# Kernel optimization log

Hardware: AMD Instinct MI355X
Metric: run time of the kernel (lower is better)

Reference implementation:

```python
import jax, jax.numpy as jnp
import numpy as np

N_NODES = 50000
N_EDGES = 800000
NUM_GRAPHS = 64
NEG_SLOPE = 0.2


def gatv2_layer(x, src, dst, Wl, bl, Wr, br, att, b_out, heads, out_ch, concat):
    # PyG GATv2Conv: x_j = lin_l(x)[src], x_i = lin_r(x)[dst]
    N = x.shape[0]
    xl = (x @ Wl + bl).reshape(N, heads, out_ch)
    xr = (x @ Wr + br).reshape(N, heads, out_ch)
    m = xl[src] + xr[dst]                                  # [E, H, C]
    e = jax.nn.leaky_relu(m, negative_slope=NEG_SLOPE)
    logits = jnp.einsum('ehc,hc->eh', e, att)              # [E, H]
    # softmax over incoming edges of each destination node
    seg_max = jax.ops.segment_max(logits, dst, num_segments=N)
    ex = jnp.exp(logits - seg_max[dst])
    denom = jax.ops.segment_sum(ex, dst, num_segments=N)
    alpha = ex / denom[dst]                                # [E, H]
    out = jax.ops.segment_sum(alpha[..., None] * xl[src], dst, num_segments=N)
    out = out.reshape(N, heads * out_ch) if concat else out.mean(axis=1)
    return out + b_out


def _forward(x, edge_index, batch,
             Wl1, bl1, Wr1, br1, att1, b1,
             Wl2, bl2, Wr2, br2, att2, b2,
             Wl3, bl3, Wr3, br3, att3, b3,
             Wm1, bm1, Wm2, bm2):
    N = x.shape[0]
    loops = jnp.arange(N, dtype=edge_index.dtype)
    src = jnp.concatenate([edge_index[0], loops])          # add_self_loops=True
    dst = jnp.concatenate([edge_index[1], loops])
    h = jax.nn.relu(gatv2_layer(x, src, dst, Wl1, bl1, Wr1, br1, att1, b1, 4, 64, True))
    h = jax.nn.relu(gatv2_layer(h, src, dst, Wl2, bl2, Wr2, br2, att2, b2, 2, 64, True))
    h = jax.nn.relu(gatv2_layer(h, src, dst, Wl3, bl3, Wr3, br3, att3, b3, 1, 64, False))
    # global_mean_pool
    sums = jax.ops.segment_sum(h, batch, num_segments=NUM_GRAPHS)
    counts = jax.ops.segment_sum(jnp.ones((N, 1), h.dtype), batch, num_segments=NUM_GRAPHS)
    pooled = sums / jnp.maximum(counts, 1.0)
    return jax.nn.relu(pooled @ Wm1 + bm1) @ Wm2 + bm2


def setup_inputs() -> dict:
    key = jax.random.key(0)
    ks = jax.random.split(key, 24)
    s = 0.05
    inp = {
        'x': jax.random.normal(ks[0], (N_NODES, 128), jnp.float32),
        'edge_index': jax.random.randint(ks[1], (2, N_EDGES), 0, N_NODES, jnp.int64),
        'batch': jnp.sort(jax.random.randint(ks[2], (N_NODES,), 0, NUM_GRAPHS, jnp.int64)),
        # conv1: in=128, heads=4, C=64
        'Wl1': jax.random.normal(ks[3], (128, 256), jnp.float32) * s,
        'bl1': jnp.zeros((256,), jnp.float32),
        'Wr1': jax.random.normal(ks[4], (128, 256), jnp.float32) * s,
        'br1': jnp.zeros((256,), jnp.float32),
        'att1': jax.random.normal(ks[5], (4, 64), jnp.float32) * s,
        'b1': jnp.zeros((256,), jnp.float32),
        # conv2: in=256, heads=2, C=64
        'Wl2': jax.random.normal(ks[6], (256, 128), jnp.float32) * s,
        'bl2': jnp.zeros((128,), jnp.float32),
        'Wr2': jax.random.normal(ks[7], (256, 128), jnp.float32) * s,
        'br2': jnp.zeros((128,), jnp.float32),
        'att2': jax.random.normal(ks[8], (2, 64), jnp.float32) * s,
        'b2': jnp.zeros((128,), jnp.float32),
        # conv3: in=128, heads=1, C=64, concat=False
        'Wl3': jax.random.normal(ks[9], (128, 64), jnp.float32) * s,
        'bl3': jnp.zeros((64,), jnp.float32),
        'Wr3': jax.random.normal(ks[10], (128, 64), jnp.float32) * s,
        'br3': jnp.zeros((64,), jnp.float32),
        'att3': jax.random.normal(ks[11], (1, 64), jnp.float32) * s,
        'b3': jnp.zeros((64,), jnp.float32),
        # MLP 64 -> 32 -> 2
        'Wm1': jax.random.normal(ks[12], (64, 32), jnp.float32) * s,
        'bm1': jnp.zeros((32,), jnp.float32),
        'Wm2': jax.random.normal(ks[13], (32, 2), jnp.float32) * s,
        'bm2': jnp.zeros((2,), jnp.float32),
    }
    return inp


def reference(x, edge_index, batch,
              Wl1, bl1, Wr1, br1, att1, b1,
              Wl2, bl2, Wr2, br2, att2, b2,
              Wl3, bl3, Wr3, br3, att3, b3,
              Wm1, bm1, Wm2, bm2):
    return _forward(x, edge_index, batch,
                    Wl1, bl1, Wr1, br1, att1, b1,
                    Wl2, bl2, Wr2, br2, att2, b2,
                    Wl3, bl3, Wr3, br3, att3, b3,
                    Wm1, bm1, Wm2, bm2)
```

## Files before the change

kernel.cpp:

```cpp
#include <hip/hip_runtime.h>


typedef __attribute__((ext_vector_type(8))) short bf16x8;
typedef __attribute__((ext_vector_type(4))) float f32x4;

#define SORT_BLOCKS 64
#define SCAN_BLOCKS 256

__device__ inline unsigned short f2bf(float f) {
    unsigned u = __float_as_uint(f);
    unsigned r = (u + 0x7fff + ((u >> 16) & 1)) >> 16;
    return (unsigned short)r;
}

__device__ inline void unpack8(uint4 a, float* d) {
    d[0] = __uint_as_float(a.x << 16); d[1] = __uint_as_float(a.x & 0xffff0000u);
    d[2] = __uint_as_float(a.y << 16); d[3] = __uint_as_float(a.y & 0xffff0000u);
    d[4] = __uint_as_float(a.z << 16); d[5] = __uint_as_float(a.z & 0xffff0000u);
    d[6] = __uint_as_float(a.w << 16); d[7] = __uint_as_float(a.w & 0xffff0000u);
}

__global__ __launch_bounds__(256) void prep_kernel(
    const float* __restrict__ x, const int* __restrict__ batch, int N, int K1,
    unsigned short* __restrict__ xb,
    const float* __restrict__ Wl1, const float* __restrict__ Wr1,
    unsigned short* __restrict__ T1l, unsigned short* __restrict__ T1r,
    const float* __restrict__ Wl2, const float* __restrict__ Wr2,
    unsigned short* __restrict__ T2l, unsigned short* __restrict__ T2r,
    const float* __restrict__ Wl3, const float* __restrict__ Wr3,
    unsigned short* __restrict__ T3l, unsigned short* __restrict__ T3r,
    int* __restrict__ deg, int* __restrict__ bound)
{
    const int gtid = blockIdx.x * 256 + threadIdx.x;
    const int gsz = (int)gridDim.x * 256;

    for (int i = gtid; i < N; i += gsz) deg[i] = 0;

    for (int n = gtid; n < N; n += gsz) {
        int bn = batch[n];
        int prev = (n == 0) ? -1 : batch[n - 1];
        for (int g = prev + 1; g <= bn; ++g) bound[g] = n;
        if (n == N - 1)
            for (int g = bn + 1; g <= 64; ++g) bound[g] = N;
    }

    {
        int n4 = (N * K1) >> 2;
        for (int i = gtid; i < n4; i += gsz) {
            float4 v = *reinterpret_cast<const float4*>(x + (size_t)i * 4);
            ushort4 o;
            o.x = f2bf(v.x); o.y = f2bf(v.y); o.z = f2bf(v.z); o.w = f2bf(v.w);
            *reinterpret_cast<ushort4*>(xb + (size_t)i * 4) = o;
        }
    }
    for (int id = gtid; id < 147456; id += gsz) {
        const float* W; unsigned short* T; int K, No, idx;
        if (id < 65536) {
            K = 128; No = 256; idx = id & 32767;
            W = (id < 32768) ? Wl1 : Wr1; T = (id < 32768) ? T1l : T1r;
        } else if (id < 131072) {
            int v = id - 65536; K = 256; No = 128; idx = v & 32767;
            W = (v < 32768) ? Wl2 : Wr2; T = (v < 32768) ? T2l : T2r;
        } else {
            int v = id - 131072; K = 128; No = 64; idx = v & 8191;
            W = (v < 8192) ? Wl3 : Wr3; T = (v < 8192) ? T3l : T3r;
        }
        int n = idx / K, k = idx - n * K;
        T[idx] = f2bf(W[(size_t)k * No + n]);
    }
}

template <int K, int NY>
__global__ __launch_bounds__(256) void gemm_slab(
    const unsigned short* __restrict__ A,
    const unsigned short* __restrict__ W0, const unsigned short* __restrict__ W1,
    const float* __restrict__ bias0, const float* __restrict__ bias1,
    unsigned short* __restrict__ OutL, unsigned short* __restrict__ OutR,
    int M)
{
    constexpr int CPR = K / 8;
    __shared__ __align__(16) char As[64 * K * 2];
    __shared__ __align__(16) char Bs[64 * 128 * 2];

    const int t = threadIdx.x;
    const int lane = t & 63;
    const int wid = t >> 6;
    const int row0 = blockIdx.x * 64;

    #pragma unroll
    for (int i = 0; i < (64 * CPR) / 256; ++i) {
        int c16 = i * 256 + t;
        int r = c16 / CPR, j = c16 % CPR;
        int gr = row0 + r; if (gr > M - 1) gr = M - 1;
        uint4 v = *reinterpret_cast<const uint4*>(A + (size_t)gr * K + j * 8);
        *reinterpret_cast<uint4*>(As + r * (2 * K) + ((j ^ (r & 7)) << 4)) = v;
    }

    const int ra = wid * 16 + (lane & 15);
    const int rowA_byte = ra * (2 * K);

    for (int z = 0; z < 2; ++z) {
        const unsigned short* Wt = z ? W1 : W0;
        const float* bias = z ? bias1 : bias0;
        unsigned short* Out = z ? OutR : OutL;
        for (int y = 0; y < NY; ++y) {
            f32x4 acc[4];
            #pragma unroll
            for (int j = 0; j < 4; ++j) acc[j] = (f32x4){0.f, 0.f, 0.f, 0.f};

            #pragma unroll
            for (int kh = 0; kh < K / 128; ++kh) {
                __syncthreads();
                #pragma unroll
                for (int i = 0; i < 4; ++i) {
                    int c16 = i * 256 + t;
                    int n = c16 >> 4, j = c16 & 15;
                    uint4 v = *reinterpret_cast<const uint4*>(
                        Wt + (size_t)(y * 64 + n) * K + kh * 128 + j * 8);
                    *reinterpret_cast<uint4*>(Bs + n * 256 + ((j ^ (n & 7)) << 4)) = v;
                }
                __syncthreads();
                #pragma unroll
                for (int ks = 0; ks < 4; ++ks) {
                    int chA = kh * 16 + ks * 4 + (lane >> 4);
                    bf16x8 a = *reinterpret_cast<const bf16x8*>(
                        As + rowA_byte + ((chA ^ (ra & 7)) << 4));
                    #pragma unroll
                    for (int j = 0; j < 4; ++j) {
                        int nb = j * 16 + (lane & 15);
                        int chB = ks * 4 + (lane >> 4);
                        bf16x8 b = *reinterpret_cast<const bf16x8*>(
                            Bs + nb * 256 + ((chB ^ (nb & 7)) << 4));
                        acc[j] = __builtin_amdgcn_mfma_f32_16x16x32_bf16(a, b, acc[j], 0, 0, 0);
                    }
                }
            }
            __syncthreads();
            #pragma unroll
            for (int j = 0; j < 4; ++j) {
                float bb = bias[y * 64 + j * 16 + (lane & 15)];
                #pragma unroll
                for (int q = 0; q < 4; ++q) {
                    int r = wid * 16 + (lane >> 4) * 4 + q;
                    int c = j * 16 + (lane & 15);
                    *reinterpret_cast<unsigned short*>(Bs + r * 128 + c * 2)
                        = f2bf(acc[j][q] + bb);
                }
            }
            __syncthreads();
            {
                int r = t >> 2, ch = t & 3;
                int gr = row0 + r;
                if (gr < M) {
                    const uint4* src = reinterpret_cast<const uint4*>(Bs + r * 128 + ch * 32);
                    uint4 v0 = src[0], v1 = src[1];
                    uint4* dst = reinterpret_cast<uint4*>(
                        Out + ((size_t)y * M + gr) * 64 + ch * 16);
                    dst[0] = v0; dst[1] = v1;
                }
            }
        }
    }
}

__global__ void hist_kernel(const int* __restrict__ ei, int E, int Etot,
                            int* __restrict__ deg)
{
    int i = blockIdx.x * blockDim.x + threadIdx.x;
    if (i >= Etot) return;
    int d = (i < E) ? ei[E + i] : (i - E);
    atomicAdd(&deg[d], 1);
}

__global__ __launch_bounds__(256) void scan1_kernel(
    const int* __restrict__ deg, int* __restrict__ blockSums, int N)
{
    __shared__ int red[256];
    const int b = blockIdx.x, t = threadIdx.x;
    const int chunk = (N + SCAN_BLOCKS - 1) / SCAN_BLOCKS;
    const int lo = b * chunk;
    const int hi = (lo + chunk < N) ? lo + chunk : N;
    int s = 0;
    for (int i = lo + t; i < hi; i += 256) s += deg[i];
    red[t] = s;
    __syncthreads();
    #pragma unroll
    for (int off = 128; off > 0; off >>= 1) {
        if (t < off) red[t] += red[t + off];
        __syncthreads();
    }
    if (t == 0) blockSums[b] = red[0];
}

__global__ __launch_bounds__(256) void scan3b_kernel(
    const int* __restrict__ deg, const int* __restrict__ blockSums,
    int* __restrict__ rowptr, int* __restrict__ cursor, int N)
{
    __shared__ int sh[256];
    const int b = blockIdx.x, t = threadIdx.x;
    const int chunk = (N + SCAN_BLOCKS - 1) / SCAN_BLOCKS;
    const int lo = b * chunk;
    const int hi = (lo + chunk < N) ? lo + chunk : N;

    sh[t] = blockSums[t];
    __syncthreads();
    for (int off = 1; off < 256; off <<= 1) {
        int u = (t >= off) ? sh[t - off] : 0;
        __syncthreads();
        sh[t] += u;
        __syncthreads();
    }
    if (b == 0 && t == 255) rowptr[N] = sh[255];
    int carry = (b == 0) ? 0 : sh[b - 1];
    __syncthreads();

    for (int j = lo; j < hi; j += 256) {
        int i = j + t;
        int v = (i < hi) ? deg[i] : 0;
        sh[t] = v;
        __syncthreads();
        for (int off = 1; off < 256; off <<= 1) {
            int u = (t >= off) ? sh[t - off] : 0;
            __syncthreads();
            sh[t] += u;
            __syncthreads();
        }
        int excl = carry + sh[t] - v;
        if (i < hi) { rowptr[i] = excl; cursor[i] = excl; }
        carry += sh[255];
        __syncthreads();
    }
}

__global__ void scatter_kernel(const int* __restrict__ ei, int E, int Etot,
                               int* __restrict__ cursor, int* __restrict__ ssrc)
{
    int i = blockIdx.x * blockDim.x + threadIdx.x;
    if (i >= Etot) return;
    int d, s;
    if (i < E) { s = ei[i]; d = ei[E + i]; }
    else       { s = i - E; d = s; }
    int pos = atomicAdd(&cursor[d], 1);
    ssrc[pos] = s;
}

__global__ __launch_bounds__(256) void dhist2_kernel(
    const int* __restrict__ rowptr, int* __restrict__ blockHist, int N)
{
    __shared__ int lh[256];
    lh[threadIdx.x] = 0;
    __syncthreads();
    const int chunk = (N + SORT_BLOCKS - 1) / SORT_BLOCKS;
    const int lo = blockIdx.x * chunk;
    const int hi = (lo + chunk < N) ? lo + chunk : N;
    for (int d = lo + threadIdx.x; d < hi; d += 256) {
        int deg = rowptr[d + 1] - rowptr[d];
        atomicAdd(&lh[deg > 255 ? 255 : deg], 1);
    }
    __syncthreads();
    blockHist[blockIdx.x * 256 + threadIdx.x] = lh[threadIdx.x];
}

__global__ __launch_bounds__(256) void dscatter2b_kernel(
    const int* __restrict__ rowptr, const int* __restrict__ blockHist,
    int* __restrict__ dperm, int N)
{
    __shared__ int sh[256];
    __shared__ int cur[256];
    const int b = blockIdx.x, t = threadIdx.x;

    int total = 0, myoff = 0;
    for (int bb = 0; bb < SORT_BLOCKS; ++bb) {
        int hv = blockHist[bb * 256 + t];
        if (bb < b) myoff += hv;
        total += hv;
    }
    sh[t] = total;
    __syncthreads();
    for (int off = 1; off < 256; off <<= 1) {
        int u = (t >= off) ? sh[t - off] : 0;
        __syncthreads();
        sh[t] += u;
        __syncthreads();
    }
    int grand = sh[255];
    cur[t] = (grand - sh[t]) + myoff;
    __syncthreads();

    const int chunk = (N + SORT_BLOCKS - 1) / SORT_BLOCKS;
    const int lo = b * chunk;
    const int hi = (lo + chunk < N) ? lo + chunk : N;
    for (int d = lo + t; d < hi; d += 256) {
        int deg = rowptr[d + 1] - rowptr[d];
        int pos = atomicAdd(&cur[deg > 255 ? 255 : deg], 1);
        dperm[pos] = d;
    }
}

template <int H, bool OUT_F32, bool OUT_BF16>
__global__ __launch_bounds__(256) void gat_fused4(
    const int* __restrict__ rowptr, const int* __restrict__ ssrc,
    const int* __restrict__ dperm,
    const unsigned short* __restrict__ xl, const unsigned short* __restrict__ xr,
    const float* __restrict__ att, const float* __restrict__ bias,
    float* __restrict__ outf, unsigned short* __restrict__ outb, int N)
{
    const int gid = blockIdx.x * 64 + (threadIdx.x >> 2);
    const int sub = threadIdx.x & 3;
    if (gid >= N * H) return;
    const int h  = gid / N;
    const int di = gid - h * N;
    const int d  = dperm[di];
    const int HC = H * 64;
    const int so = sub * 16;

    const unsigned short* xlh = xl + (size_t)h * N * 64;

    float xrv[16], attv[16], acc[16];
    {
        const unsigned short* pr = xr + ((size_t)h * N + d) * 64 + so;
        uint4 v0 = *reinterpret_cast<const uint4*>(pr);
        uint4 v1 = *reinterpret_cast<const uint4*>(pr + 8);
        unpack8(v0, xrv); unpack8(v1, xrv + 8);
        const float* pa = att + h * 64 + so;
        #pragma unroll
        for (int k = 0; k < 16; k += 4) {
            float4 w = *reinterpret_cast<const float4*>(pa + k);
            attv[k] = w.x; attv[k+1] = w.y; attv[k+2] = w.z; attv[k+3] = w.w;
        }
    }
    #pragma unroll
    for (int k = 0; k < 16; ++k) acc[k] = 0.f;
    float M = -3.0e38f, S = 0.f;

    const int begin = rowptr[d], end = rowptr[d + 1];
    uint4 c0, c1;
    {
        const unsigned short* pl = xlh + (size_t)ssrc[begin] * 64 + so;
        c0 = *reinterpret_cast<const uint4*>(pl);
        c1 = *reinterpret_cast<const uint4*>(pl + 8);
    }
    for (int e = begin; e < end; ++e) {
        uint4 n0, n1;
        const bool more = (e + 1 < end);
        if (more) {
            const unsigned short* pl = xlh + (size_t)ssrc[e + 1] * 64 + so;
            n0 = *reinterpret_cast<const uint4*>(pl);
            n1 = *reinterpret_cast<const uint4*>(pl + 8);
        }
        float cur[16];
        unpack8(c0, cur);
        unpack8(c1, cur + 8);
        float p = 0.f;
        #pragma unroll
        for (int k = 0; k < 16; ++k) {
            float v = cur[k] + xrv[k];
            v = fmaxf(v, 0.2f * v);
            p = fmaf(v, attv[k], p);
        }
        p += __shfl_xor(p, 1);
        p += __shfl_xor(p, 2);
        float nM = fmaxf(M, p);
        float scale = __expf(M - nM);
        float w = __expf(p - nM);
        S = fmaf(S, scale, w);
        #pragma unroll
        for (int k = 0; k < 16; ++k) acc[k] = fmaf(acc[k], scale, w * cur[k]);
        M = nM;
        if (more) { c0 = n0; c1 = n1; }
    }
    float inv = 1.f / S;
    const float* pb = bias + h * 64 + so;
    #pragma unroll
    for (int k = 0; k < 16; ++k) {
        float val = fmaf(acc[k], inv, pb[k]);
        acc[k] = val > 0.f ? val : 0.f;
    }
    size_t ob = (size_t)d * HC + h * 64 + so;
    if (OUT_F32) {
        #pragma unroll
        for (int k = 0; k < 16; k += 4) {
            float4 v = {acc[k], acc[k+1], acc[k+2], acc[k+3]};
            *reinterpret_cast<float4*>(outf + ob + k) = v;
        }
    }
    if (OUT_BF16) {
        unsigned pk[8];
        #pragma unroll
        for (int k = 0; k < 8; ++k)
            pk[k] = (unsigned)f2bf(acc[2*k]) | ((unsigned)f2bf(acc[2*k+1]) << 16);
        uint4 lo = {pk[0], pk[1], pk[2], pk[3]};
        uint4 hi = {pk[4], pk[5], pk[6], pk[7]};
        *reinterpret_cast<uint4*>(outb + ob) = lo;
        *reinterpret_cast<uint4*>(outb + ob + 8) = hi;
    }
}

__global__ __launch_bounds__(1024) void graph_pool_mlp(
    const float* __restrict__ h3, const int* __restrict__ bound,
    const float* __restrict__ Wm1, const float* __restrict__ bm1,
    const float* __restrict__ Wm2, const float* __restrict__ bm2,
    float* __restrict__ out)
{
    __shared__ float sh[1024];
    __shared__ float pooled[64];
    __shared__ float hidden[32];
    const int g = blockIdx.x;
    const int t = threadIdx.x;
    const int ch = t & 63;
    const int slot = t >> 6;
    const int lo = bound[g];
    const int hi = bound[g + 1];

    float acc = 0.f;
    #pragma unroll 4
    for (int n = lo + slot; n < hi; n += 16)
        acc += h3[(size_t)n * 64 + ch];
    sh[t] = acc;
    __syncthreads();
    #pragma unroll
    for (int off = 512; off >= 64; off >>= 1) {
        if (t < off) sh[t] += sh[t + off];
        __syncthreads();
    }
    if (t < 64) {
        float cnt = (float)(hi - lo);
        cnt = cnt > 1.f ? cnt : 1.f;
        pooled[t] = sh[t] / cnt;
    }
    __syncthreads();
    if (t < 32) {
        float a = bm1[t];
        #pragma unroll
        for (int k = 0; k < 64; ++k) a = fmaf(pooled[k], Wm1[k * 32 + t], a);
        hidden[t] = a > 0.f ? a : 0.f;
    }
    __syncthreads();
    if (t < 2) {
        float a = bm2[t];
        #pragma unroll
        for (int j = 0; j < 32; ++j) a = fmaf(hidden[j], Wm2[j * 2 + t], a);
        out[g * 2 + t] = a;
    }
}

static void run_layer(const unsigned short* Xb, int K, int H,
                      const float* bl, const float* br,
                      const float* att, const float* bias_out,
                      const unsigned short* Wtl, const unsigned short* Wtr,
                      const int* rowptr, const int* ssrc, const int* dperm, int N,
                      unsigned short* xl, unsigned short* xr,
                      float* houtf, unsigned short* houtb,
                      hipStream_t stream)
{
    int gblocks = (N + 63) / 64;
    if (K == 128 && H == 4)
        gemm_slab<128, 4><<<gblocks, 256, 0, stream>>>(Xb, Wtl, Wtr, bl, br, xl, xr, N);
    else if (K == 256)
        gemm_slab<256, 2><<<gblocks, 256, 0, stream>>>(Xb, Wtl, Wtr, bl, br, xl, xr, N);
    else
        gemm_slab<128, 1><<<gblocks, 256, 0, stream>>>(Xb, Wtl, Wtr, bl, br, xl, xr, N);

    int ngroups = N * H;
    int blocks = (ngroups + 63) / 64;
    if (H == 4)
        gat_fused4<4, false, true><<<blocks, 256, 0, stream>>>(
            rowptr, ssrc, dperm, xl, xr, att, bias_out, houtf, houtb, N);
    else if (H == 2)
        gat_fused4<2, false, true><<<blocks, 256, 0, stream>>>(
            rowptr, ssrc, dperm, xl, xr, att, bias_out, houtf, houtb, N);
    else
        gat_fused4<1, true, false><<<blocks, 256, 0, stream>>>(
            rowptr, ssrc, dperm, xl, xr, att, bias_out, houtf, houtb, N);
}

extern "C" void kernel_launch(void* const* d_in, const int* in_sizes, int n_in,
                              void* d_out, int out_size, void* d_ws, size_t ws_size,
                              hipStream_t stream)
{
    const float* x    = (const float*)d_in[0];
    const int*   ei   = (const int*)d_in[1];
    const int*   batch= (const int*)d_in[2];
    const float* Wl1 = (const float*)d_in[3];
    const float* bl1 = (const float*)d_in[4];
    const float* Wr1 = (const float*)d_in[5];
    const float* br1 = (const float*)d_in[6];
    const float* att1= (const float*)d_in[7];
    const float* b1  = (const float*)d_in[8];
    const float* Wl2 = (const float*)d_in[9];
    const float* bl2 = (const float*)d_in[10];
    const float* Wr2 = (const float*)d_in[11];
    const float* br2 = (const float*)d_in[12];
    const float* att2= (const float*)d_in[13];
    const float* b2  = (const float*)d_in[14];
    const float* Wl3 = (const float*)d_in[15];
    const float* bl3 = (const float*)d_in[16];
    const float* Wr3 = (const float*)d_in[17];
    const float* br3 = (const float*)d_in[18];
    const float* att3= (const float*)d_in[19];
    const float* b3  = (const float*)d_in[20];
    const float* Wm1 = (const float*)d_in[21];
    const float* bm1 = (const float*)d_in[22];
    const float* Wm2 = (const float*)d_in[23];
    const float* bm2 = (const float*)d_in[24];

    const int N    = in_sizes[2];
    const int E    = in_sizes[1] / 2;
    const int Etot = E + N;
    const int K1   = in_sizes[0] / N;

    char* wsb = (char*)d_ws;
    size_t o = 0;
    auto alloc = [&](size_t bytes) { char* p = wsb + o; o += (bytes + 255) & ~(size_t)255; return p; };
    unsigned short* xl    = (unsigned short*)alloc((size_t)N * 256 * 2);
    unsigned short* xr    = (unsigned short*)alloc((size_t)N * 256 * 2);
    unsigned short* xb    = (unsigned short*)alloc((size_t)N * K1 * 2);
    unsigned short* h1b   = (unsigned short*)alloc((size_t)N * 256 * 2);
    unsigned short* h2b   = (unsigned short*)alloc((size_t)N * 128 * 2);
    float*          h3f   = (float*)alloc((size_t)N * 64 * 4);
    int*   deg    = (int*)alloc((size_t)N * 4);
    int*   rowptr = (int*)alloc((size_t)(N + 1) * 4);
    int*   cursor = (int*)alloc((size_t)N * 4);
    int*   ssrc   = (int*)alloc((size_t)Etot * 4);
    int*   dperm  = (int*)alloc((size_t)N * 4);
    int*   bound  = (int*)alloc(65 * 4);
    int*   blockHist = (int*)alloc((size_t)SORT_BLOCKS * 256 * 4);
    int*   blockSums = (int*)alloc((size_t)SCAN_BLOCKS * 4);
    unsigned short* Wt1l = (unsigned short*)alloc(128 * 256 * 2);
    unsigned short* Wt1r = (unsigned short*)alloc(128 * 256 * 2);
    unsigned short* Wt2l = (unsigned short*)alloc(256 * 128 * 2);
    unsigned short* Wt2r = (unsigned short*)alloc(256 * 128 * 2);
    unsigned short* Wt3l = (unsigned short*)alloc(128 * 64 * 2);
    unsigned short* Wt3r = (unsigned short*)alloc(128 * 64 * 2);
    (void)ws_size; (void)n_in; (void)out_size;

    prep_kernel<<<1024, 256, 0, stream>>>(
        x, batch, N, K1, xb,
        Wl1, Wr1, Wt1l, Wt1r, Wl2, Wr2, Wt2l, Wt2r, Wl3, Wr3, Wt3l, Wt3r,
        deg, bound);

    hist_kernel<<<(Etot + 255) / 256, 256, 0, stream>>>(ei, E, Etot, deg);
    scan1_kernel<<<SCAN_BLOCKS, 256, 0, stream>>>(deg, blockSums, N);
    scan3b_kernel<<<SCAN_BLOCKS, 256, 0, stream>>>(deg, blockSums, rowptr, cursor, N);
    scatter_kernel<<<(Etot + 255) / 256, 256, 0, stream>>>(ei, E, Etot, cursor, ssrc);
    dhist2_kernel<<<SORT_BLOCKS, 256, 0, stream>>>(rowptr, blockHist, N);
    dscatter2b_kernel<<<SORT_BLOCKS, 256, 0, stream>>>(rowptr, blockHist, dperm, N);

    run_layer(xb, K1, 4, bl1, br1, att1, b1, Wt1l, Wt1r,
              rowptr, ssrc, dperm, N, xl, xr, nullptr, h1b, stream);
    run_layer(h1b, 256, 2, bl2, br2, att2, b2, Wt2l, Wt2r,
              rowptr, ssrc, dperm, N, xl, xr, nullptr, h2b, stream);
    run_layer(h2b, 128, 1, bl3, br3, att3, b3, Wt3l, Wt3r,
              rowptr, ssrc, dperm, N, xl, xr, h3f, nullptr, stream);

    graph_pool_mlp<<<64, 1024, 0, stream>>>(
        h3f, bound, Wm1, bm1, Wm2, bm2, (float*)d_out);
}
```

Baseline: 322.6 us.

## Prefetch GEMM weights into registers, fold degree histogram into scan, remap GAT blocks

The GEMM slab kernel flattens its z/y/kh loops into one stage loop and loads the next weight tile into registers while the current tile feeds the MFMAs, so global latency overlaps compute. The degree histogram used for the degree sort is now built inside the scan kernel, which removes the separate dhist2 launch and its second pass over rowptr. The sort now uses 256 blocks instead of 64. The GAT aggregation grid interleaves heads across neighbouring block IDs, so blocks running together share the same destination nodes and their edge lists, which should improve cache reuse. The risks are the extra registers held for prefetching and a larger blockHist that each dscatter block must sum over.

```diff
diff --git a/kernel.cpp b/kernel.cpp
--- a/kernel.cpp
+++ b/kernel.cpp
@@ -4,7 +4,6 @@
 typedef __attribute__((ext_vector_type(8))) short bf16x8;
 typedef __attribute__((ext_vector_type(4))) float f32x4;
 
-#define SORT_BLOCKS 64
 #define SCAN_BLOCKS 256
 
 __device__ inline unsigned short f2bf(float f) {
@@ -79,6 +78,8 @@
     int M)
 {
     constexpr int CPR = K / 8;
+    constexpr int KH  = K / 128;
+    constexpr int NST = 2 * NY * KH;
     __shared__ __align__(16) char As[64 * K * 2];
     __shared__ __align__(16) char Bs[64 * 128 * 2];
 
@@ -99,42 +100,57 @@
     const int ra = wid * 16 + (lane & 15);
     const int rowA_byte = ra * (2 * K);
 
-    for (int z = 0; z < 2; ++z) {
+    uint4 wreg[4];
+    auto loadW = [&](int s) {
+        int z = s / (NY * KH); int rr = s - z * (NY * KH);
+        int y = rr / KH; int kh = rr - y * KH;
         const unsigned short* Wt = z ? W1 : W0;
-        const float* bias = z ? bias1 : bias0;
-        unsigned short* Out = z ? OutR : OutL;
-        for (int y = 0; y < NY; ++y) {
-            f32x4 acc[4];
+        #pragma unroll
+        for (int u = 0; u < 4; ++u) {
+            int c = u * 256 + t;
+            int n = c >> 4, j = c & 15;
+            wreg[u] = *reinterpret_cast<const uint4*>(
+                Wt + (size_t)(y * 64 + n) * K + kh * 128 + j * 8);
+        }
+    };
+    loadW(0);
+
+    f32x4 acc[4];
+    #pragma unroll
+    for (int j = 0; j < 4; ++j) acc[j] = (f32x4){0.f, 0.f, 0.f, 0.f};
+
+    for (int s = 0; s < NST; ++s) {
+        int z = s / (NY * KH); int rr = s - z * (NY * KH);
+        int y = rr / KH; int kh = rr - y * KH;
+
+        __syncthreads();
+        #pragma unroll
+        for (int u = 0; u < 4; ++u) {
+            int c = u * 256 + t;
+            int n = c >> 4, j = c & 15;
+            *reinterpret_cast<uint4*>(Bs + n * 256 + ((j ^ (n & 7)) << 4)) = wreg[u];
+        }
+        __syncthreads();
+        if (s + 1 < NST) loadW(s + 1);
+
+        #pragma unroll
+        for (int ks = 0; ks < 4; ++ks) {
+            int chA = kh * 16 + ks * 4 + (lane >> 4);
+            bf16x8 a = *reinterpret_cast<const bf16x8*>(
+                As + rowA_byte + ((chA ^ (ra & 7)) << 4));
             #pragma unroll
-            for (int j = 0; j < 4; ++j) acc[j] = (f32x4){0.f, 0.f, 0.f, 0.f};
-
-            #pragma unroll
-            for (int kh = 0; kh < K / 128; ++kh) {
-                __syncthreads();
-                #pragma unroll
-                for (int i = 0; i < 4; ++i) {
-                    int c16 = i * 256 + t;
-                    int n = c16 >> 4, j = c16 & 15;
-                    uint4 v = *reinterpret_cast<const uint4*>(
-                        Wt + (size_t)(y * 64 + n) * K + kh * 128 + j * 8);
-                    *reinterpret_cast<uint4*>(Bs + n * 256 + ((j ^ (n & 7)) << 4)) = v;
-                }
-                __syncthreads();
-                #pragma unroll
-                for (int ks = 0; ks < 4; ++ks) {
-                    int chA = kh * 16 + ks * 4 + (lane >> 4);
-                    bf16x8 a = *reinterpret_cast<const bf16x8*>(
-                        As + rowA_byte + ((chA ^ (ra & 7)) << 4));
-                    #pragma unroll
-                    for (int j = 0; j < 4; ++j) {
-                        int nb = j * 16 + (lane & 15);
-                        int chB = ks * 4 + (lane >> 4);
-                        bf16x8 b = *reinterpret_cast<const bf16x8*>(
-                            Bs + nb * 256 + ((chB ^ (nb & 7)) << 4));
-                        acc[j] = __builtin_amdgcn_mfma_f32_16x16x32_bf16(a, b, acc[j], 0, 0, 0);
-                    }
-                }
+            for (int j = 0; j < 4; ++j) {
+                int nb = j * 16 + (lane & 15);
+                int chB = ks * 4 + (lane >> 4);
+                bf16x8 b = *reinterpret_cast<const bf16x8*>(
+                    Bs + nb * 256 + ((chB ^ (nb & 7)) << 4));
+                acc[j] = __builtin_amdgcn_mfma_f32_16x16x32_bf16(a, b, acc[j], 0, 0, 0);
             }
+        }
+
+        if (kh == KH - 1) {
+            unsigned short* Out = z ? OutR : OutL;
+            const float* bias = z ? bias1 : bias0;
             __syncthreads();
             #pragma unroll
             for (int j = 0; j < 4; ++j) {
@@ -146,18 +162,17 @@
                     *reinterpret_cast<unsigned short*>(Bs + r * 128 + c * 2)
                         = f2bf(acc[j][q] + bb);
                 }
+                acc[j] = (f32x4){0.f, 0.f, 0.f, 0.f};
             }
             __syncthreads();
-            {
-                int r = t >> 2, ch = t & 3;
-                int gr = row0 + r;
-                if (gr < M) {
-                    const uint4* src = reinterpret_cast<const uint4*>(Bs + r * 128 + ch * 32);
-                    uint4 v0 = src[0], v1 = src[1];
-                    uint4* dst = reinterpret_cast<uint4*>(
-                        Out + ((size_t)y * M + gr) * 64 + ch * 16);
-                    dst[0] = v0; dst[1] = v1;
-                }
+            int r = t >> 2, ch = t & 3;
+            int gr = row0 + r;
+            if (gr < M) {
+                const uint4* src = reinterpret_cast<const uint4*>(Bs + r * 128 + ch * 32);
+                uint4 v0 = src[0], v1 = src[1];
+                uint4* dst = reinterpret_cast<uint4*>(
+                    Out + ((size_t)y * M + gr) * 64 + ch * 16);
+                dst[0] = v0; dst[1] = v1;
             }
         }
     }
@@ -194,14 +209,17 @@
 
 __global__ __launch_bounds__(256) void scan3b_kernel(
     const int* __restrict__ deg, const int* __restrict__ blockSums,
-    int* __restrict__ rowptr, int* __restrict__ cursor, int N)
+    int* __restrict__ rowptr, int* __restrict__ cursor,
+    int* __restrict__ blockHist, int N)
 {
     __shared__ int sh[256];
+    __shared__ int lh[256];
     const int b = blockIdx.x, t = threadIdx.x;
     const int chunk = (N + SCAN_BLOCKS - 1) / SCAN_BLOCKS;
     const int lo = b * chunk;
     const int hi = (lo + chunk < N) ? lo + chunk : N;
 
+    lh[t] = 0;
     sh[t] = blockSums[t];
     __syncthreads();
     for (int off = 1; off < 256; off <<= 1) {
@@ -226,10 +244,14 @@
             __syncthreads();
         }
         int excl = carry + sh[t] - v;
-        if (i < hi) { rowptr[i] = excl; cursor[i] = excl; }
+        if (i < hi) {
+            rowptr[i] = excl; cursor[i] = excl;
+            atomicAdd(&lh[v > 255 ? 255 : v], 1);
+        }
         carry += sh[255];
         __syncthreads();
     }
+    blockHist[b * 256 + t] = lh[t];
 }
 
 __global__ void scatter_kernel(const int* __restrict__ ei, int E, int Etot,
@@ -244,23 +266,6 @@
     ssrc[pos] = s;
 }
 
-__global__ __launch_bounds__(256) void dhist2_kernel(
-    const int* __restrict__ rowptr, int* __restrict__ blockHist, int N)
-{
-    __shared__ int lh[256];
-    lh[threadIdx.x] = 0;
-    __syncthreads();
-    const int chunk = (N + SORT_BLOCKS - 1) / SORT_BLOCKS;
-    const int lo = blockIdx.x * chunk;
-    const int hi = (lo + chunk < N) ? lo + chunk : N;
-    for (int d = lo + threadIdx.x; d < hi; d += 256) {
-        int deg = rowptr[d + 1] - rowptr[d];
-        atomicAdd(&lh[deg > 255 ? 255 : deg], 1);
-    }
-    __syncthreads();
-    blockHist[blockIdx.x * 256 + threadIdx.x] = lh[threadIdx.x];
-}
-
 __global__ __launch_bounds__(256) void dscatter2b_kernel(
     const int* __restrict__ rowptr, const int* __restrict__ blockHist,
     int* __restrict__ dperm, int N)
@@ -270,7 +275,7 @@
     const int b = blockIdx.x, t = threadIdx.x;
 
     int total = 0, myoff = 0;
-    for (int bb = 0; bb < SORT_BLOCKS; ++bb) {
+    for (int bb = 0; bb < SCAN_BLOCKS; ++bb) {
         int hv = blockHist[bb * 256 + t];
         if (bb < b) myoff += hv;
         total += hv;
@@ -287,7 +292,7 @@
     cur[t] = (grand - sh[t]) + myoff;
     __syncthreads();
 
-    const int chunk = (N + SORT_BLOCKS - 1) / SORT_BLOCKS;
+    const int chunk = (N + SCAN_BLOCKS - 1) / SCAN_BLOCKS;
     const int lo = b * chunk;
     const int hi = (lo + chunk < N) ? lo + chunk : N;
     for (int d = lo + t; d < hi; d += 256) {
@@ -303,13 +308,25 @@
     const int* __restrict__ dperm,
     const unsigned short* __restrict__ xl, const unsigned short* __restrict__ xr,
     const float* __restrict__ att, const float* __restrict__ bias,
-    float* __restrict__ outf, unsigned short* __restrict__ outb, int N)
-{
-    const int gid = blockIdx.x * 64 + (threadIdx.x >> 2);
+    float* __restrict__ outf, unsigned short* __restrict__ outb,
+    int N, int BPH)
+{
+    const int bid = blockIdx.x;
+    int h, j;
+    if (H == 4) {
+        h = (bid & 7) >> 1;
+        j = ((bid >> 3) << 1) | (bid & 1);
+    } else if (H == 2) {
+        h = (bid & 7) >> 2;
+        j = ((bid >> 3) << 2) | (bid & 3);
+    } else {
+        h = 0;
+        j = bid;
+    }
+    if (j >= BPH) return;
+    const int di = j * 64 + (threadIdx.x >> 2);
     const int sub = threadIdx.x & 3;
-    if (gid >= N * H) return;
-    const int h  = gid / N;
-    const int di = gid - h * N;
+    if (di >= N) return;
     const int d  = dperm[di];
     const int HC = H * 64;
     const int so = sub * 16;
@@ -461,17 +478,19 @@
     else
         gemm_slab<128, 1><<<gblocks, 256, 0, stream>>>(Xb, Wtl, Wtr, bl, br, xl, xr, N);
 
-    int ngroups = N * H;
-    int blocks = (ngroups + 63) / 64;
-    if (H == 4)
-        gat_fused4<4, false, true><<<blocks, 256, 0, stream>>>(
-            rowptr, ssrc, dperm, xl, xr, att, bias_out, houtf, houtb, N);
-    else if (H == 2)
-        gat_fused4<2, false, true><<<blocks, 256, 0, stream>>>(
-            rowptr, ssrc, dperm, xl, xr, att, bias_out, houtf, houtb, N);
-    else
-        gat_fused4<1, true, false><<<blocks, 256, 0, stream>>>(
-            rowptr, ssrc, dperm, xl, xr, att, bias_out, houtf, houtb, N);
+    int BPH = (N + 63) / 64;
+    if (H == 4) {
+        int grid = ((BPH * 4 + 7) / 8) * 8;
+        gat_fused4<4, false, true><<<grid, 256, 0, stream>>>(
+            rowptr, ssrc, dperm, xl, xr, att, bias_out, houtf, houtb, N, BPH);
+    } else if (H == 2) {
+        int grid = ((BPH * 2 + 7) / 8) * 8;
+        gat_fused4<2, false, true><<<grid, 256, 0, stream>>>(
+            rowptr, ssrc, dperm, xl, xr, att, bias_out, houtf, houtb, N, BPH);
+    } else {
+        gat_fused4<1, true, false><<<BPH, 256, 0, stream>>>(
+            rowptr, ssrc, dperm, xl, xr, att, bias_out, houtf, houtb, N, BPH);
+    }
 }
 
 extern "C" void kernel_launch(void* const* d_in, const int* in_sizes, int n_in,
@@ -524,7 +543,7 @@
     int*   ssrc   = (int*)alloc((size_t)Etot * 4);
     int*   dperm  = (int*)alloc((size_t)N * 4);
     int*   bound  = (int*)alloc(65 * 4);
-    int*   blockHist = (int*)alloc((size_t)SORT_BLOCKS * 256 * 4);
+    int*   blockHist = (int*)alloc((size_t)SCAN_BLOCKS * 256 * 4);
     int*   blockSums = (int*)alloc((size_t)SCAN_BLOCKS * 4);
     unsigned short* Wt1l = (unsigned short*)alloc(128 * 256 * 2);
     unsigned short* Wt1r = (unsigned short*)alloc(128 * 256 * 2);
@@ -541,10 +560,9 @@
 
     hist_kernel<<<(Etot + 255) / 256, 256, 0, stream>>>(ei, E, Etot, deg);
     scan1_kernel<<<SCAN_BLOCKS, 256, 0, stream>>>(deg, blockSums, N);
-    scan3b_kernel<<<SCAN_BLOCKS, 256, 0, stream>>>(deg, blockSums, rowptr, cursor, N);
+    scan3b_kernel<<<SCAN_BLOCKS, 256, 0, stream>>>(deg, blockSums, rowptr, cursor, blockHist, N);
     scatter_kernel<<<(Etot + 255) / 256, 256, 0, stream>>>(ei, E, Etot, cursor, ssrc);
-    dhist2_kernel<<<SORT_BLOCKS, 256, 0, stream>>>(rowptr, blockHist, N);
-    dscatter2b_kernel<<<SORT_BLOCKS, 256, 0, stream>>>(rowptr, blockHist, dperm, N);
+    dscatter2b_kernel<<<SCAN_BLOCKS, 256, 0, stream>>>(rowptr, blockHist, dperm, N);
 
     run_layer(xb, K1, 4, bl1, br1, att1, b1, Wt1l, Wt1r,
               rowptr, ssrc, dperm, N, xl, xr, nullptr, h1b, stream);
```

Result: slower. 366.7 us (+13.7%).
